# Optimization experiments

Hardware: AMD Instinct MI355X
Metric: run time of the kernel (lower is better)

## Reference

```python
import jax, jax.numpy as jnp
import numpy as np

N_USERS = 1024
N_ITEMS = 2048
N = N_USERS + N_ITEMS          # 3072 total nodes
D = 128                        # latent_dim_rec
L = 3                          # n_layers
K = [64, 64, 64]               # top-k per layer for getMaskAdj
GAMMA = 0.2                    # residual weight on svd embeddings
X_SCALE = 1.0                  # delta
B = 8192                       # batch of (user, item) pairs


def setup_inputs() -> dict:
    key = jax.random.key(0)
    ks = jax.random.split(key, 9)
    # normalized-adjacency-like dense graph: nonnegative, row sums ~ 1
    A = jax.random.uniform(ks[0], (N, N), dtype=jnp.float32) * (2.0 / N)
    user_emb = jax.random.normal(ks[1], (N_USERS, D), dtype=jnp.float32)
    item_emb = jax.random.normal(ks[2], (N_ITEMS, D), dtype=jnp.float32)
    user_emb0 = jax.random.normal(ks[3], (N_USERS, D), dtype=jnp.float32)
    item_emb0 = jax.random.normal(ks[4], (N_ITEMS, D), dtype=jnp.float32)
    vector_u = jax.random.uniform(ks[5], (1, N), dtype=jnp.float32)
    vector_v = jax.random.uniform(ks[6], (1, N), dtype=jnp.float32)
    users = jax.random.randint(ks[7], (B,), 0, N_USERS)
    items = jax.random.randint(ks[8], (B,), 0, N_ITEMS)
    return {
        "users": users, "items": items, "A": A,
        "user_emb": user_emb, "item_emb": item_emb,
        "user_emb0": user_emb0, "item_emb0": item_emb0,
        "vector_u": vector_u, "vector_v": vector_v,
    }


def topk_mask(M, k):
    """Keep top-k entries per row of M, zero elsewhere (getMaskAdj)."""
    vals, idx = jax.lax.top_k(M, k)          # [N,k], [N,k]
    rows = jnp.arange(M.shape[0])[:, None]
    return jnp.zeros_like(M).at[rows, idx].set(vals)


def _computer(A, user_emb, item_emb, user_emb0, item_emb0, vector_u, vector_v):
    all_emb = jnp.concatenate([user_emb, item_emb], axis=0)      # [N,D]
    all_emb0 = jnp.concatenate([user_emb0, item_emb0], axis=0)   # [N,D]
    u = vector_u[0]  # [N]
    v = vector_v[0]  # [N]

    # ---- computAttention: w_k = u A^k v for k = 0..L (A^0 = I via A_0=eye) ----
    w_list = [jnp.dot(u, v)]
    powers = []           # A^1 .. A^L (g_droped progression)
    Ak = A
    for layer in range(L):
        powers.append(Ak)
        w_list.append(jnp.dot(u, Ak @ v))
        if layer < L - 1:
            Ak = A @ Ak   # g_droped = Graph @ A_k
    w = jnp.stack(w_list)                 # [L+1]
    w = w / jnp.sum(w)
    attention_weight = jax.nn.softmax(w)  # softmax(dim=0)

    # ---- getMaskAdj: top-k masked powers ----
    A_list = [topk_mask(powers[l], K[l]) if K[l] != 0 else powers[l] for l in range(L)]

    # ---- layer-wise propagation with attention-weighted accumulation ----
    emb0 = all_emb
    light_out = X_SCALE * attention_weight[0] * all_emb
    for layer in range(L):
        e = A_list[layer] @ emb0 + GAMMA * all_emb0   # SpMM + residual
        light_out = light_out + X_SCALE * attention_weight[layer + 1] * e
    users_all = light_out[:N_USERS]
    items_all = light_out[N_USERS:]
    return users_all, items_all


def reference(users, items, A, user_emb, item_emb, user_emb0, item_emb0, vector_u, vector_v):
    users_all, items_all = _computer(A, user_emb, item_emb, user_emb0, item_emb0, vector_u, vector_v)
    u_e = users_all[users]   # [B,D]
    i_e = items_all[items]   # [B,D]
    return jnp.sum(u_e * i_e, axis=1)  # [B]
```

## Files before the change

### kernel.cpp

```cpp
#include <hip/hip_runtime.h>
#include <hip/hip_fp8.h>
#include <math.h>

#define NN 3072
#define NU 1024
#define NI 2048
#define DD 128
#define BB 8192
#define GAMMA_F 0.2f

#define SCALE_A 524288.0f
#define F8SCALE2 1.9073486328125e-06f
#define DESCALE38 3.637978807091713e-12f

#define KBLK ((size_t)NN * 64)

typedef __attribute__((ext_vector_type(4))) float f32x4;
typedef __attribute__((ext_vector_type(16))) float f32x16;
typedef __attribute__((ext_vector_type(4))) int i32x4;
typedef __attribute__((ext_vector_type(8))) int i32x8;

static __device__ inline unsigned short bf16bits(float x) {
  union { unsigned u; float f; } cv;
  cv.f = x;
  unsigned r = cv.u + 0x7fff + ((cv.u >> 16) & 1);
  return (unsigned short)(r >> 16);
}

static __device__ inline unsigned pk4_f8(float a, float b, float c, float d) {
#if defined(__has_builtin)
#if __has_builtin(__builtin_amdgcn_cvt_pk_fp8_f32)
  int p = __builtin_amdgcn_cvt_pk_fp8_f32(a, b, 0, false);
  p = __builtin_amdgcn_cvt_pk_fp8_f32(c, d, p, true);
  return (unsigned)p;
#else
  return (unsigned)__hip_fp8_e4m3(a).__x | ((unsigned)__hip_fp8_e4m3(b).__x << 8) |
         ((unsigned)__hip_fp8_e4m3(c).__x << 16) |
         ((unsigned)__hip_fp8_e4m3(d).__x << 24);
#endif
#else
  return (unsigned)__hip_fp8_e4m3(a).__x | ((unsigned)__hip_fp8_e4m3(b).__x << 8) |
         ((unsigned)__hip_fp8_e4m3(c).__x << 16) |
         ((unsigned)__hip_fp8_e4m3(d).__x << 24);
#endif
}

static __device__ inline void atomAddF(float* p, float v) {
#if defined(__has_builtin)
#if __has_builtin(__builtin_amdgcn_global_atomic_fadd_f32)
  __builtin_amdgcn_global_atomic_fadd_f32(
      (__attribute__((address_space(1))) float*)p, v);
#else
  unsafeAtomicAdd(p, v);
#endif
#else
  unsafeAtomicAdd(p, v);
#endif
}

static __device__ inline float block_sum(float s, float* red4) {
  int tid = threadIdx.x;
  for (int off = 32; off; off >>= 1) s += __shfl_down(s, off, 64);
  if ((tid & 63) == 0) red4[tid >> 6] = s;
  __syncthreads();
  return red4[0] + red4[1] + red4[2] + red4[3];
}

static __device__ inline float row_dot_f32(const float* __restrict__ a,
                                           const float* __restrict__ b,
                                           float* red4) {
  const float4* ap = (const float4*)a;
  const float4* bp = (const float4*)b;
  float s = 0.f;
  for (int j = threadIdx.x; j < NN / 4; j += 256) {
    float4 x = ap[j], y = bp[j];
    s += x.x * y.x + x.y * y.y + x.z * y.z + x.w * y.w;
  }
  return block_sum(s, red4);
}

static __device__ inline void load48_bf(const unsigned short* __restrict__ b0,
                                        int parts, int row, int lane,
                                        float* f) {
  const uint4* r0 = (const uint4*)(b0 + (size_t)row * NN);
#pragma unroll
  for (int j = 0; j < 6; ++j) {
    uint4 q = r0[lane + j * 64];
    unsigned uu[4] = {q.x, q.y, q.z, q.w};
#pragma unroll
    for (int e = 0; e < 4; ++e) {
      f[j * 8 + e * 2] = __uint_as_float(uu[e] << 16);
      f[j * 8 + e * 2 + 1] = __uint_as_float(uu[e] & 0xffff0000u);
    }
  }
  for (int p = 1; p < parts; ++p) {
    const uint4* rp = (const uint4*)(b0 + (size_t)p * NN * NN + (size_t)row * NN);
#pragma unroll
    for (int j = 0; j < 6; ++j) {
      uint4 q = rp[lane + j * 64];
      unsigned uu[4] = {q.x, q.y, q.z, q.w};
#pragma unroll
      for (int e = 0; e < 4; ++e) {
        f[j * 8 + e * 2] += __uint_as_float(uu[e] << 16);
        f[j * 8 + e * 2 + 1] += __uint_as_float(uu[e] & 0xffff0000u);
      }
    }
  }
}

static __device__ inline void load48_f32(const float* __restrict__ A, int row,
                                         int lane, float* f) {
  const float4* r0 = (const float4*)(A + (size_t)row * NN);
#pragma unroll
  for (int j = 0; j < 12; ++j) {
    float4 a = r0[lane + j * 64];
    f[j * 4 + 0] = a.x; f[j * 4 + 1] = a.y;
    f[j * 4 + 2] = a.z; f[j * 4 + 3] = a.w;
  }
}

static __device__ void select_compact(const float* f, int lane, float descale,
                                      int bf, int* __restrict__ outCnt,
                                      int* __restrict__ outIdx,
                                      float* __restrict__ outVal) {
  unsigned bor = 0, band = 0xffffffffu;
#pragma unroll
  for (int r = 0; r < 48; ++r) {
    unsigned k = __float_as_uint(f[r]);
    bor |= k; band &= k;
  }
  for (int off = 32; off; off >>= 1) {
    bor |= (unsigned)__shfl_xor((int)bor, off, 64);
    band &= (unsigned)__shfl_xor((int)band, off, 64);
  }
  unsigned diff = bor ^ band;
  int hi = diff ? (31 - __clz(diff)) : 16;
  if (hi < 16) hi = 16;
  if (hi > 30) hi = 30;
  unsigned t = band & ~((2u << hi) - 1u);

  int b = hi;
  while (b >= 17) {
    unsigned base = 1u << (b - 1);
    unsigned cand1 = t | base;
    unsigned cand2 = t | (base << 1);
    unsigned cand3 = cand2 | base;
    int c1 = 0, c2 = 0, c3 = 0;
#pragma unroll
    for (int r = 0; r < 48; ++r) {
      unsigned k = __float_as_uint(f[r]);
      c1 += (k >= cand1) ? 1 : 0;
      c2 += (k >= cand2) ? 1 : 0;
      c3 += (k >= cand3) ? 1 : 0;
    }
    for (int off = 32; off; off >>= 1) {
      c1 += __shfl_xor(c1, off, 64);
      c2 += __shfl_xor(c2, off, 64);
      c3 += __shfl_xor(c3, off, 64);
    }
    if (c3 >= 64) t = cand3;
    else if (c2 >= 64) t = cand2;
    else if (c1 >= 64) t = cand1;
    b -= 2;
  }
  if (b == 16) {
    unsigned cand = t | (1u << 16);
    int c = 0;
#pragma unroll
    for (int r = 0; r < 48; ++r) c += (__float_as_uint(f[r]) >= cand) ? 1 : 0;
    for (int off = 32; off; off >>= 1) c += __shfl_xor(c, off, 64);
    if (c >= 64) t = cand;
  }

  int basec = 0;
#pragma unroll
  for (int r = 0; r < 48; ++r) {
    bool keep = __float_as_uint(f[r]) >= t;
    unsigned long long m = __ballot(keep);
    if (keep) {
      int pos = basec + __popcll(m & ((1ull << lane) - 1ull));
      if (pos < 128) {
        int col = bf ? ((r >> 3) * 512 + lane * 8 + (r & 7))
                     : ((r >> 2) * 256 + lane * 4 + (r & 3));
        outIdx[pos] = col << 7;
        outVal[pos] = f[r] * descale;
      }
    }
    basec += __popcll(m);
  }
  if (lane == 0) *outCnt = basec < 128 ? basec : 128;
}

__global__ __launch_bounds__(256) void prep(
    const float* __restrict__ A, const float* __restrict__ vu,
    const float* __restrict__ vv, unsigned char* __restrict__ Af8,
    unsigned char* __restrict__ Atf8, float* __restrict__ y1,
    float* __restrict__ s1, const float* __restrict__ uemb,
    const float* __restrict__ iemb, float* __restrict__ allE) {
  __shared__ float sh[64 * 65 + 512];
  const int bid = blockIdx.x;
  const int t = threadIdx.x;
  if (bid >= 2304) {
    int idx = (bid - 2304) * 256 + t;
    int e = idx * 4;
    float4 v = (e < NU * DD) ? *(const float4*)(uemb + e)
                             : *(const float4*)(iemb + (e - NU * DD));
    *(float4*)(allE + e) = v;
    return;
  }
  const int bx = (bid % 48) * 64, by = (bid / 48) * 64;
  const int rr = t >> 4;
  const int c4 = (t & 15) * 4;
  for (int it = 0; it < 4; ++it) {
    int r = rr + it * 16;
    float4 val = *(const float4*)(A + (size_t)(by + r) * NN + bx + c4);
    sh[r * 65 + c4] = val.x; sh[r * 65 + c4 + 1] = val.y;
    sh[r * 65 + c4 + 2] = val.z; sh[r * 65 + c4 + 3] = val.w;
  }
  __syncthreads();
  {
    int row = t >> 2, ch = t & 3;
    const float* sp = &sh[row * 65 + ch * 16];
    uint4 w;
    w.x = pk4_f8(sp[0] * SCALE_A, sp[1] * SCALE_A, sp[2] * SCALE_A,
                 sp[3] * SCALE_A);
    w.y = pk4_f8(sp[4] * SCALE_A, sp[5] * SCALE_A, sp[6] * SCALE_A,
                 sp[7] * SCALE_A);
    w.z = pk4_f8(sp[8] * SCALE_A, sp[9] * SCALE_A, sp[10] * SCALE_A,
                 sp[11] * SCALE_A);
    w.w = pk4_f8(sp[12] * SCALE_A, sp[13] * SCALE_A, sp[14] * SCALE_A,
                 sp[15] * SCALE_A);
    *(uint4*)(Af8 + (size_t)(bx >> 6) * KBLK + (size_t)(by + row) * 64 +
              ch * 16) = w;
  }
  {
    int c = t >> 2, ch = t & 3;
    float v[16];
#pragma unroll
    for (int e = 0; e < 16; ++e) v[e] = sh[(ch * 16 + e) * 65 + c];
    uint4 w;
    w.x = pk4_f8(v[0] * SCALE_A, v[1] * SCALE_A, v[2] * SCALE_A,
                 v[3] * SCALE_A);
    w.y = pk4_f8(v[4] * SCALE_A, v[5] * SCALE_A, v[6] * SCALE_A,
                 v[7] * SCALE_A);
    w.z = pk4_f8(v[8] * SCALE_A, v[9] * SCALE_A, v[10] * SCALE_A,
                 v[11] * SCALE_A);
    w.w = pk4_f8(v[12] * SCALE_A, v[13] * SCALE_A, v[14] * SCALE_A,
                 v[15] * SCALE_A);
    *(uint4*)(Atf8 + (size_t)(by >> 6) * KBLK + (size_t)(bx + c) * 64 +
              ch * 16) = w;
  }
  const int q = t >> 6;
  const int l = t & 63;
  float sy = 0.f, ss_ = 0.f;
  for (int i = 0; i < 16; ++i) {
    int c = q * 16 + i;
    sy += sh[l * 65 + c] * vv[bx + c];
    ss_ += vu[by + c] * sh[c * 65 + l];
  }
  float* red = sh + 64 * 65;
  red[q * 64 + l] = sy;
  red[256 + q * 64 + l] = ss_;
  __syncthreads();
  if (t < 64) {
    float v4 = red[t] + red[64 + t] + red[128 + t] + red[192 + t];
    atomAddF(&y1[by + t], v4);
  } else if (t < 128) {
    int cc = t - 64;
    float v4 = red[256 + cc] + red[256 + 64 + cc] + red[256 + 128 + cc] +
               red[256 + 192 + cc];
    atomAddF(&s1[bx + cc], v4);
  }
}

static __device__ inline i32x8 ldfragL(const char* p) {
  i32x4 lo = *(const i32x4*)p;
  i32x4 hi = *(const i32x4*)(p + 1024);
  return (i32x8){lo.x, lo.y, lo.z, lo.w, hi.x, hi.y, hi.z, hi.w};
}

__global__ __launch_bounds__(256) void gemm_f8(
    const unsigned char* __restrict__ Ag,
    const unsigned char* __restrict__ Btg,
    unsigned short* __restrict__ Cg) {
  __shared__ char smem[3][24576];
  const int wg = blockIdx.x;
  const int xcd = wg & 7;
  const int idx = wg >> 3;
  const int bxi = xcd * 2 + (idx & 1);
  const int byi = idx >> 1;
  const int rowBase = byi * 192, colBase = bxi * 192;

  const int t = threadIdx.x;
  const int w = t >> 6, l = t & 63;
  const int wr = w >> 1, wc = w & 1;
  const int r32 = l & 31, hh = l >> 5;

  f32x16 acc[3][3];
#pragma unroll
  for (int i = 0; i < 3; ++i)
#pragma unroll
    for (int j = 0; j < 3; ++j)
#pragma unroll
      for (int e = 0; e < 16; ++e) acc[i][j][e] = 0.f;

  const unsigned char* aT = Ag + (size_t)rowBase * 64;
  const unsigned char* bT = Btg + (size_t)colBase * 64;
  const int laneOff = r32 * 64 + hh * 32;

#define STAGE(kt, b)                                                        \
  {                                                                         \
    const size_t kOff = (size_t)(kt) * KBLK;                                \
    _Pragma("unroll") for (int r_ = 0; r_ < 6; ++r_) {                      \
      int q_ = r_ * 4 + w;                                                  \
      int qq_ = q_ < 12 ? q_ : q_ - 12;                                     \
      int s_ = qq_ >> 1, h_ = qq_ & 1;                                      \
      const unsigned char* g_ = ((q_ < 12) ? aT : bT) + kOff +              \
                                (size_t)(s_ * 32) * 64 + laneOff + h_ * 16; \
      __builtin_amdgcn_global_load_lds(                                     \
          (const __attribute__((address_space(1))) unsigned*)g_,            \
          (__attribute__((address_space(3))) unsigned*)(smem[b] +           \
                                                        q_ * 1024),         \
          16, 0, 0);                                                        \
    }                                                                       \
  }

  const int nt = NN / 64;
  STAGE(0, 0);
  STAGE(1, 1);
  for (int kt = 0; kt < nt; ++kt) {
    if (kt < nt - 1) {
      asm volatile("s_waitcnt vmcnt(6)" ::: "memory");
    } else {
      asm volatile("s_waitcnt vmcnt(0)" ::: "memory");
    }
    __builtin_amdgcn_s_barrier();
    __builtin_amdgcn_sched_barrier(0);
    const char* sb = smem[kt % 3];
    i32x8 af[3], bfr[3];
#pragma unroll
    for (int i = 0; i < 3; ++i)
      af[i] = ldfragL(sb + (wr * 3 + i) * 2048 + l * 16);
#pragma unroll
    for (int j = 0; j < 3; ++j)
      bfr[j] = ldfragL(sb + 12288 + (wc * 3 + j) * 2048 + l * 16);
    if (kt + 2 < nt) STAGE(kt + 2, (kt + 2) % 3);
    __builtin_amdgcn_s_setprio(1);
#pragma unroll
    for (int i = 0; i < 3; ++i)
#pragma unroll
      for (int j = 0; j < 3; ++j)
        acc[i][j] = __builtin_amdgcn_mfma_scale_f32_32x32x64_f8f6f4(
            af[i], bfr[j], acc[i][j], 0, 0, 0, 127, 0, 127);
    __builtin_amdgcn_s_setprio(0);
    __builtin_amdgcn_sched_barrier(0);
  }
#undef STAGE

#pragma unroll
  for (int i = 0; i < 3; ++i) {
    int rb = rowBase + wr * 96 + i * 32 + 4 * hh;
#pragma unroll
    for (int j = 0; j < 3; ++j) {
      int cc = colBase + wc * 96 + j * 32 + r32;
#pragma unroll
      for (int reg = 0; reg < 16; ++reg) {
        int rr = rb + (reg & 3) + 8 * (reg >> 2);
        Cg[(size_t)rr * NN + cc] = bf16bits(acc[i][j][reg]);
      }
    }
  }
}

__global__ __launch_bounds__(256) void post1(
    const unsigned short* __restrict__ C, int parts,
    const float* __restrict__ A, const float* __restrict__ y1,
    unsigned char* __restrict__ A2f8, int* __restrict__ cnts1,
    int* __restrict__ tIdx1, float* __restrict__ tVal1,
    float* __restrict__ tvec) {
  const int bid = blockIdx.x;
  const int t = threadIdx.x;
  if (bid < 768) {
    int row = bid * 4 + (t >> 6);
    int lane = t & 63;
    float f[48];
    load48_bf(C, parts, row, lane, f);
#pragma unroll
    for (int j = 0; j < 6; ++j) {
      uint2 w;
      w.x = pk4_f8(f[j * 8 + 0] * F8SCALE2, f[j * 8 + 1] * F8SCALE2,
                   f[j * 8 + 2] * F8SCALE2, f[j * 8 + 3] * F8SCALE2);
      w.y = pk4_f8(f[j * 8 + 4] * F8SCALE2, f[j * 8 + 5] * F8SCALE2,
                   f[j * 8 + 6] * F8SCALE2, f[j * 8 + 7] * F8SCALE2);
      size_t addr = (size_t)(j * 8 + (lane >> 3)) * KBLK +
                    (size_t)row * 64 + (lane & 7) * 8;
      *(uint2*)(A2f8 + addr) = w;
    }
    select_compact(f, lane, DESCALE38, 1, &cnts1[row],
                   tIdx1 + (size_t)row * 128, tVal1 + (size_t)row * 128);
  } else {
    int row = (bid - 768) * 4 + (t >> 6);
    int lane = t & 63;
    const float4* rp = (const float4*)(A + (size_t)row * NN);
    const float4* yp = (const float4*)y1;
    float s = 0.f;
#pragma unroll
    for (int j = 0; j < 12; ++j) {
      float4 a = rp[lane + j * 64];
      float4 y = yp[lane + j * 64];
      s += a.x * y.x + a.y * y.y + a.z * y.z + a.w * y.w;
    }
    for (int off = 32; off; off >>= 1) s += __shfl_down(s, off, 64);
    if (lane == 0) tvec[row] = s;
  }
}

__global__ __launch_bounds__(256) void sel02(
    const unsigned short* __restrict__ C, int parts,
    const float* __restrict__ A, int* __restrict__ cnt0,
    int* __restrict__ idx0, float* __restrict__ val0,
    int* __restrict__ cnt2, int* __restrict__ idx2,
    float* __restrict__ val2, const float* __restrict__ vu,
    const float* __restrict__ vv, const float* __restrict__ y1,
    const float* __restrict__ s1, const float* __restrict__ tvec,
    float* __restrict__ wacc) {
  __shared__ float red4[4];
  const int bid = blockIdx.x;
  const int t = threadIdx.x;
  if (bid == 1536) {
    float w0 = row_dot_f32(vu, vv, red4);  __syncthreads();
    float w1 = row_dot_f32(vu, y1, red4);  __syncthreads();
    float w2 = row_dot_f32(s1, y1, red4);  __syncthreads();
    float w3 = row_dot_f32(s1, tvec, red4);
    if (t == 0) { wacc[0] = w0; wacc[1] = w1; wacc[2] = w2; wacc[3] = w3; }
    return;
  }
  const int w = t >> 6, lane = t & 63;
  const int row = (bid >> 1) * 4 + w;
  float f[48];
  if ((bid & 1) == 0) {
    load48_bf(C, parts, row, lane, f);
    select_compact(f, lane, DESCALE38, 1, &cnt2[row],
                   idx2 + (size_t)row * 128, val2 + (size_t)row * 128);
  } else {
    load48_f32(A, row, lane, f);
    select_compact(f, lane, 1.0f, 0, &cnt0[row],
                   idx0 + (size_t)row * 128, val0 + (size_t)row * 128);
  }
}

__global__ __launch_bounds__(256) void gather_light(
    const float* __restrict__ allE, const float* __restrict__ uemb0,
    const float* __restrict__ iemb0, const float* __restrict__ wacc,
    const int* __restrict__ cnt0, const int* __restrict__ idx0,
    const float* __restrict__ val0, const int* __restrict__ cnts1,
    const int* __restrict__ tIdx1, const float* __restrict__ tVal1,
    const int* __restrict__ cnt2, const int* __restrict__ idx2,
    const float* __restrict__ val2, float* __restrict__ lightOut) {
  __shared__ int li[4][384];
  __shared__ float lv[4][384];
  const int t = threadIdx.x;
  const int w = t >> 6, lane = t & 63;
  const int row = blockIdx.x * 4 + w;

  float w0 = wacc[0], w1 = wacc[1], w2 = wacc[2], w3 = wacc[3];
  float ss = w0 + w1 + w2 + w3;
  w0 /= ss; w1 /= ss; w2 /= ss; w3 /= ss;
  float m = fmaxf(fmaxf(w0, w1), fmaxf(w2, w3));
  float ex0 = expf(w0 - m), ex1 = expf(w1 - m), ex2 = expf(w2 - m),
        ex3 = expf(w3 - m);
  float se = ex0 + ex1 + ex2 + ex3;
  float aw0 = ex0 / se, aw1 = ex1 / se, aw2 = ex2 / se, aw3 = ex3 / se;
  float aw4 = GAMMA_F * (aw1 + aw2 + aw3);

  const int c0 = cnt0[row], c1 = cnts1[row], c2 = cnt2[row];
  const int p0 = (c0 + 7) & ~7, p1 = (c1 + 7) & ~7, p2 = (c2 + 7) & ~7;
  int* Li = li[w];
  float* Lv = lv[w];
  const size_t rb = (size_t)row * 128;
  for (int k = lane; k < p0; k += 64) {
    bool in = k < c0;
    Li[k] = in ? idx0[rb + k] : 0;
    Lv[k] = in ? aw1 * val0[rb + k] : 0.f;
  }
  for (int k = lane; k < p1; k += 64) {
    bool in = k < c1;
    Li[p0 + k] = in ? tIdx1[rb + k] : 0;
    Lv[p0 + k] = in ? aw2 * tVal1[rb + k] : 0.f;
  }
  for (int k = lane; k < p2; k += 64) {
    bool in = k < c2;
    Li[p0 + p1 + k] = in ? idx2[rb + k] : 0;
    Lv[p0 + p1 + k] = in ? aw3 * val2[rb + k] : 0.f;
  }

  const int ct = p0 + p1 + p2;
  const float2* E2 = (const float2*)allE;
  float ax = 0.f, ay = 0.f, bx_ = 0.f, by_ = 0.f;
  for (int k = 0; k < ct; k += 8) {
    int i0 = Li[k + 0], i1 = Li[k + 1], i2 = Li[k + 2], i3 = Li[k + 3];
    int i4 = Li[k + 4], i5 = Li[k + 5], i6 = Li[k + 6], i7 = Li[k + 7];
    float v0 = Lv[k + 0], v1 = Lv[k + 1], v2 = Lv[k + 2], v3 = Lv[k + 3];
    float v4 = Lv[k + 4], v5 = Lv[k + 5], v6 = Lv[k + 6], v7 = Lv[k + 7];
    float2 g0 = E2[(i0 >> 1) + lane];
    float2 g1 = E2[(i1 >> 1) + lane];
    float2 g2 = E2[(i2 >> 1) + lane];
    float2 g3 = E2[(i3 >> 1) + lane];
    float2 g4 = E2[(i4 >> 1) + lane];
    float2 g5 = E2[(i5 >> 1) + lane];
    float2 g6 = E2[(i6 >> 1) + lane];
    float2 g7 = E2[(i7 >> 1) + lane];
    ax += v0 * g0.x; ay += v0 * g0.y;
    bx_ += v1 * g1.x; by_ += v1 * g1.y;
    ax += v2 * g2.x; ay += v2 * g2.y;
    bx_ += v3 * g3.x; by_ += v3 * g3.y;
    ax += v4 * g4.x; ay += v4 * g4.y;
    bx_ += v5 * g5.x; by_ += v5 * g5.y;
    ax += v6 * g6.x; ay += v6 * g6.y;
    bx_ += v7 * g7.x; by_ += v7 * g7.y;
  }
  float2 sE = E2[((size_t)row << 6) + lane];
  float2 e0 = (row < NU)
                  ? ((const float2*)uemb0)[(size_t)row * 64 + lane]
                  : ((const float2*)iemb0)[(size_t)(row - NU) * 64 + lane];
  float ox = (ax + bx_) + aw0 * sE.x + aw4 * e0.x;
  float oy = (ay + by_) + aw0 * sE.y + aw4 * e0.y;
  float2 o; o.x = ox; o.y = oy;
  ((float2*)lightOut)[(size_t)row * 64 + lane] = o;
}

__global__ __launch_bounds__(256) void out_dot(const int* __restrict__ users,
                                               const int* __restrict__ items,
                                               const float* __restrict__ lightOut,
                                               float* __restrict__ out) {
  int b = blockIdx.x * 4 + (threadIdx.x >> 6);
  int lane = threadIdx.x & 63;
  const float* up = lightOut + (size_t)users[b] * DD;
  const float* ip = lightOut + (size_t)(NU + items[b]) * DD;
  float s = up[lane] * ip[lane] + up[lane + 64] * ip[lane + 64];
  for (int off = 32; off; off >>= 1) s += __shfl_down(s, off, 64);
  if (lane == 0) out[b] = s;
}

extern "C" void kernel_launch(void* const* d_in, const int* in_sizes, int n_in,
                              void* d_out, int out_size, void* d_ws,
                              size_t ws_size, hipStream_t stream) {
  const int* users = (const int*)d_in[0];
  const int* items = (const int*)d_in[1];
  const float* A = (const float*)d_in[2];
  const float* uemb = (const float*)d_in[3];
  const float* iemb = (const float*)d_in[4];
  const float* uemb0 = (const float*)d_in[5];
  const float* iemb0 = (const float*)d_in[6];
  const float* vu = (const float*)d_in[7];
  const float* vv = (const float*)d_in[8];
  float* out = (float*)d_out;

  char* ws = (char*)d_ws;
  size_t off = 0;
  auto alloc = [&](size_t bytes) -> void* {
    void* p = ws + off;
    off += (bytes + 255) & ~(size_t)255;
    return p;
  };
  unsigned char* Af8 = (unsigned char*)alloc((size_t)NN * NN);
  unsigned char* Atf8 = (unsigned char*)alloc((size_t)NN * NN);
  unsigned char* A2f8 = (unsigned char*)alloc((size_t)NN * NN);
  float* y1 = (float*)alloc((size_t)NN * 4);
  float* s1 = (float*)alloc((size_t)NN * 4);
  float* tvec = (float*)alloc((size_t)NN * 4);
  float* wacc = (float*)alloc(256);
  int* cnts1 = (int*)alloc((size_t)NN * 4);
  int* tIdx1 = (int*)alloc((size_t)NN * 128 * 4);
  float* tVal1 = (float*)alloc((size_t)NN * 128 * 4);
  float* lightOut = (float*)alloc((size_t)NN * DD * 4);
  int* cnt0 = (int*)alloc((size_t)NN * 4);
  int* cnt2 = (int*)alloc((size_t)NN * 4);
  float* allE = (float*)alloc((size_t)NN * DD * 4);

  const size_t LSTB = (size_t)NN * 128 * 4;
  int* idx0 = (int*)(Atf8);
  float* val0 = (float*)(Atf8 + LSTB);
  int* idx2 = (int*)(Atf8 + 2 * LSTB);
  float* val2 = (float*)(Atf8 + 3 * LSTB);

  unsigned short* C = (unsigned short*)alloc((size_t)NN * NN * 2);

  hipMemsetAsync(y1, 0, (size_t)2 * NN * 4, stream);
  prep<<<2688, 256, 0, stream>>>(A, vu, vv, Af8, Atf8, y1, s1, uemb, iemb,
                                 allE);
  gemm_f8<<<256, 256, 0, stream>>>(Af8, Atf8, C);
  post1<<<1536, 256, 0, stream>>>(C, 1, A, y1, A2f8, cnts1, tIdx1, tVal1,
                                  tvec);
  gemm_f8<<<256, 256, 0, stream>>>(A2f8, Atf8, C);
  sel02<<<1537, 256, 0, stream>>>(C, 1, A, cnt0, idx0, val0, cnt2, idx2,
                                  val2, vu, vv, y1, s1, tvec, wacc);
  gather_light<<<768, 256, 0, stream>>>(allE, uemb0, iemb0, wacc, cnt0, idx0,
                                        val0, cnts1, tIdx1, tVal1, cnt2, idx2,
                                        val2, lightOut);
  out_dot<<<BB / 4, 256, 0, stream>>>(users, items, lightOut, out);
}
```

Measured before the change: 239.9 us.

## Split K across two wave groups in FP8 GEMM with LDS reduction

The FP8 GEMM block grows from 4 to 8 waves. Two groups of four waves each handle alternating 64-wide K tiles with their own triple-buffered LDS staging. At the end, the second group writes its accumulators to shared memory and the first group adds them before storing bf16 output. This raises the number of waves per CU to hide memory and MFMA latency, since there are only 256 blocks. The cost is doubled LDS use (about 144KB per block), a barrier-synchronised reduction through LDS, and higher register pressure under launch_bounds 512.

```diff
diff --git a/kernel.cpp b/kernel.cpp
--- a/kernel.cpp
+++ b/kernel.cpp
@@ -279,11 +279,11 @@
   return (i32x8){lo.x, lo.y, lo.z, lo.w, hi.x, hi.y, hi.z, hi.w};
 }
 
-__global__ __launch_bounds__(256) void gemm_f8(
+__global__ __launch_bounds__(512) void gemm_f8(
     const unsigned char* __restrict__ Ag,
     const unsigned char* __restrict__ Btg,
     unsigned short* __restrict__ Cg) {
-  __shared__ char smem[3][24576];
+  __shared__ char smem[2][3][24576];
   const int wg = blockIdx.x;
   const int xcd = wg & 7;
   const int idx = wg >> 3;
@@ -293,7 +293,9 @@
 
   const int t = threadIdx.x;
   const int w = t >> 6, l = t & 63;
-  const int wr = w >> 1, wc = w & 1;
+  const int kp = w >> 2;
+  const int wq = w & 3;
+  const int wr = wq >> 1, wc = wq & 1;
   const int r32 = l & 31, hh = l >> 5;
 
   f32x16 acc[3][3];
@@ -312,61 +314,85 @@
   {                                                                         \
     const size_t kOff = (size_t)(kt) * KBLK;                                \
     _Pragma("unroll") for (int r_ = 0; r_ < 6; ++r_) {                      \
-      int q_ = r_ * 4 + w;                                                  \
+      int q_ = r_ * 4 + wq;                                                 \
       int qq_ = q_ < 12 ? q_ : q_ - 12;                                     \
       int s_ = qq_ >> 1, h_ = qq_ & 1;                                      \
       const unsigned char* g_ = ((q_ < 12) ? aT : bT) + kOff +              \
                                 (size_t)(s_ * 32) * 64 + laneOff + h_ * 16; \
       __builtin_amdgcn_global_load_lds(                                     \
           (const __attribute__((address_space(1))) unsigned*)g_,            \
-          (__attribute__((address_space(3))) unsigned*)(smem[b] +           \
+          (__attribute__((address_space(3))) unsigned*)(smem[kp][b] +       \
                                                         q_ * 1024),         \
           16, 0, 0);                                                        \
     }                                                                       \
   }
 
-  const int nt = NN / 64;
-  STAGE(0, 0);
-  STAGE(1, 1);
-  for (int kt = 0; kt < nt; ++kt) {
-    if (kt < nt - 1) {
+  const int ni = 24;
+  STAGE(kp, 0);
+  STAGE(2 + kp, 1);
+  for (int i = 0; i < ni; ++i) {
+    if (i < ni - 1) {
       asm volatile("s_waitcnt vmcnt(6)" ::: "memory");
     } else {
       asm volatile("s_waitcnt vmcnt(0)" ::: "memory");
     }
     __builtin_amdgcn_s_barrier();
     __builtin_amdgcn_sched_barrier(0);
-    const char* sb = smem[kt % 3];
+    const char* sb = smem[kp][i % 3];
     i32x8 af[3], bfr[3];
 #pragma unroll
-    for (int i = 0; i < 3; ++i)
-      af[i] = ldfragL(sb + (wr * 3 + i) * 2048 + l * 16);
+    for (int ii = 0; ii < 3; ++ii)
+      af[ii] = ldfragL(sb + (wr * 3 + ii) * 2048 + l * 16);
 #pragma unroll
     for (int j = 0; j < 3; ++j)
       bfr[j] = ldfragL(sb + 12288 + (wc * 3 + j) * 2048 + l * 16);
-    if (kt + 2 < nt) STAGE(kt + 2, (kt + 2) % 3);
+    if (i + 2 < ni) STAGE(2 * (i + 2) + kp, (i + 2) % 3);
     __builtin_amdgcn_s_setprio(1);
 #pragma unroll
-    for (int i = 0; i < 3; ++i)
+    for (int ii = 0; ii < 3; ++ii)
 #pragma unroll
       for (int j = 0; j < 3; ++j)
-        acc[i][j] = __builtin_amdgcn_mfma_scale_f32_32x32x64_f8f6f4(
-            af[i], bfr[j], acc[i][j], 0, 0, 0, 127, 0, 127);
+        acc[ii][j] = __builtin_amdgcn_mfma_scale_f32_32x32x64_f8f6f4(
+            af[ii], bfr[j], acc[ii][j], 0, 0, 0, 127, 0, 127);
     __builtin_amdgcn_s_setprio(0);
     __builtin_amdgcn_sched_barrier(0);
   }
 #undef STAGE
 
-#pragma unroll
-  for (int i = 0; i < 3; ++i) {
-    int rb = rowBase + wr * 96 + i * 32 + 4 * hh;
-#pragma unroll
-    for (int j = 0; j < 3; ++j) {
-      int cc = colBase + wc * 96 + j * 32 + r32;
-#pragma unroll
-      for (int reg = 0; reg < 16; ++reg) {
-        int rr = rb + (reg & 3) + 8 * (reg >> 2);
-        Cg[(size_t)rr * NN + cc] = bf16bits(acc[i][j][reg]);
+  float* mbase = (float*)&smem[0][0][0];
+  if (kp == 1) {
+    float* dst = mbase + (size_t)wq * 9216;
+#pragma unroll
+    for (int i = 0; i < 3; ++i)
+#pragma unroll
+      for (int j = 0; j < 3; ++j) {
+        float* p = dst + (i * 3 + j) * 1024 + l * 16;
+#pragma unroll
+        for (int e = 0; e < 16; ++e) p[e] = acc[i][j][e];
+      }
+  }
+  __syncthreads();
+  if (kp == 0) {
+    const float* src = mbase + (size_t)wq * 9216;
+#pragma unroll
+    for (int i = 0; i < 3; ++i)
+#pragma unroll
+      for (int j = 0; j < 3; ++j) {
+        const float* p = src + (i * 3 + j) * 1024 + l * 16;
+#pragma unroll
+        for (int e = 0; e < 16; ++e) acc[i][j][e] += p[e];
+      }
+#pragma unroll
+    for (int i = 0; i < 3; ++i) {
+      int rb = rowBase + wr * 96 + i * 32 + 4 * hh;
+#pragma unroll
+      for (int j = 0; j < 3; ++j) {
+        int cc = colBase + wc * 96 + j * 32 + r32;
+#pragma unroll
+        for (int reg = 0; reg < 16; ++reg) {
+          int rr = rb + (reg & 3) + 8 * (reg >> 2);
+          Cg[(size_t)rr * NN + cc] = bf16bits(acc[i][j][reg]);
+        }
       }
     }
   }
@@ -589,10 +615,10 @@
   hipMemsetAsync(y1, 0, (size_t)2 * NN * 4, stream);
   prep<<<2688, 256, 0, stream>>>(A, vu, vv, Af8, Atf8, y1, s1, uemb, iemb,
                                  allE);
-  gemm_f8<<<256, 256, 0, stream>>>(Af8, Atf8, C);
+  gemm_f8<<<256, 512, 0, stream>>>(Af8, Atf8, C);
   post1<<<1536, 256, 0, stream>>>(C, 1, A, y1, A2f8, cnts1, tIdx1, tVal1,
                                   tvec);
-  gemm_f8<<<256, 256, 0, stream>>>(A2f8, Atf8, C);
+  gemm_f8<<<256, 512, 0, stream>>>(A2f8, Atf8, C);
   sel02<<<1537, 256, 0, stream>>>(C, 1, A, cnt0, idx0, val0, cnt2, idx2,
                                   val2, vu, vv, y1, s1, tvec, wacc);
   gather_light<<<768, 256, 0, stream>>>(allE, uemb0, iemb0, wacc, cnt0, idx0,
```

Result: no change. 240.2 us (+0.1%).

## Split FP8 GEMM K dimension in two to double workgroup count

Applied to the files above, without the earlier changes.

The FP8 matrix-power GEMM now splits the 3072-long K loop into two halves, launching 512 workgroups instead of 256. Each half writes its own bf16 partial result buffer, and the consumer kernels sum the two parts. The goal is to fill more of the GPU's compute units, since 256 workgroups underuse the device. In exchange it doubles the intermediate C memory traffic and adds rounding of two bf16 partials. Launch bounds are also raised to two blocks per CU.

```diff
diff --git a/kernel.cpp b/kernel.cpp
--- a/kernel.cpp
+++ b/kernel.cpp
@@ -279,7 +279,7 @@
   return (i32x8){lo.x, lo.y, lo.z, lo.w, hi.x, hi.y, hi.z, hi.w};
 }
 
-__global__ __launch_bounds__(256) void gemm_f8(
+__global__ __launch_bounds__(256, 2) void gemm_f8(
     const unsigned char* __restrict__ Ag,
     const unsigned char* __restrict__ Btg,
     unsigned short* __restrict__ Cg) {
@@ -288,7 +288,8 @@
   const int xcd = wg & 7;
   const int idx = wg >> 3;
   const int bxi = xcd * 2 + (idx & 1);
-  const int byi = idx >> 1;
+  const int byi = (idx >> 1) & 15;
+  const int z = idx >> 5;
   const int rowBase = byi * 192, colBase = bxi * 192;
 
   const int t = threadIdx.x;
@@ -307,6 +308,7 @@
   const unsigned char* aT = Ag + (size_t)rowBase * 64;
   const unsigned char* bT = Btg + (size_t)colBase * 64;
   const int laneOff = r32 * 64 + hh * 32;
+  const int kt0 = z * 24;
 
 #define STAGE(kt, b)                                                        \
   {                                                                         \
@@ -325,38 +327,39 @@
     }                                                                       \
   }
 
-  const int nt = NN / 64;
-  STAGE(0, 0);
-  STAGE(1, 1);
-  for (int kt = 0; kt < nt; ++kt) {
-    if (kt < nt - 1) {
+  const int ni = 24;
+  STAGE(kt0, 0);
+  STAGE(kt0 + 1, 1);
+  for (int i = 0; i < ni; ++i) {
+    if (i < ni - 1) {
       asm volatile("s_waitcnt vmcnt(6)" ::: "memory");
     } else {
       asm volatile("s_waitcnt vmcnt(0)" ::: "memory");
     }
     __builtin_amdgcn_s_barrier();
     __builtin_amdgcn_sched_barrier(0);
-    const char* sb = smem[kt % 3];
+    const char* sb = smem[i % 3];
     i32x8 af[3], bfr[3];
 #pragma unroll
-    for (int i = 0; i < 3; ++i)
-      af[i] = ldfragL(sb + (wr * 3 + i) * 2048 + l * 16);
+    for (int ii = 0; ii < 3; ++ii)
+      af[ii] = ldfragL(sb + (wr * 3 + ii) * 2048 + l * 16);
 #pragma unroll
     for (int j = 0; j < 3; ++j)
       bfr[j] = ldfragL(sb + 12288 + (wc * 3 + j) * 2048 + l * 16);
-    if (kt + 2 < nt) STAGE(kt + 2, (kt + 2) % 3);
+    if (i + 2 < ni) STAGE(kt0 + i + 2, (i + 2) % 3);
     __builtin_amdgcn_s_setprio(1);
 #pragma unroll
-    for (int i = 0; i < 3; ++i)
+    for (int ii = 0; ii < 3; ++ii)
 #pragma unroll
       for (int j = 0; j < 3; ++j)
-        acc[i][j] = __builtin_amdgcn_mfma_scale_f32_32x32x64_f8f6f4(
-            af[i], bfr[j], acc[i][j], 0, 0, 0, 127, 0, 127);
+        acc[ii][j] = __builtin_amdgcn_mfma_scale_f32_32x32x64_f8f6f4(
+            af[ii], bfr[j], acc[ii][j], 0, 0, 0, 127, 0, 127);
     __builtin_amdgcn_s_setprio(0);
     __builtin_amdgcn_sched_barrier(0);
   }
 #undef STAGE
 
+  unsigned short* Cout = Cg + (size_t)z * NN * NN;
 #pragma unroll
   for (int i = 0; i < 3; ++i) {
     int rb = rowBase + wr * 96 + i * 32 + 4 * hh;
@@ -366,7 +369,7 @@
 #pragma unroll
       for (int reg = 0; reg < 16; ++reg) {
         int rr = rb + (reg & 3) + 8 * (reg >> 2);
-        Cg[(size_t)rr * NN + cc] = bf16bits(acc[i][j][reg]);
+        Cout[(size_t)rr * NN + cc] = bf16bits(acc[i][j][reg]);
       }
     }
   }
@@ -584,16 +587,16 @@
   int* idx2 = (int*)(Atf8 + 2 * LSTB);
   float* val2 = (float*)(Atf8 + 3 * LSTB);
 
-  unsigned short* C = (unsigned short*)alloc((size_t)NN * NN * 2);
+  unsigned short* C = (unsigned short*)alloc((size_t)2 * NN * NN * 2);
 
   hipMemsetAsync(y1, 0, (size_t)2 * NN * 4, stream);
   prep<<<2688, 256, 0, stream>>>(A, vu, vv, Af8, Atf8, y1, s1, uemb, iemb,
                                  allE);
-  gemm_f8<<<256, 256, 0, stream>>>(Af8, Atf8, C);
-  post1<<<1536, 256, 0, stream>>>(C, 1, A, y1, A2f8, cnts1, tIdx1, tVal1,
+  gemm_f8<<<512, 256, 0, stream>>>(Af8, Atf8, C);
+  post1<<<1536, 256, 0, stream>>>(C, 2, A, y1, A2f8, cnts1, tIdx1, tVal1,
                                   tvec);
-  gemm_f8<<<256, 256, 0, stream>>>(A2f8, Atf8, C);
-  sel02<<<1537, 256, 0, stream>>>(C, 1, A, cnt0, idx0, val0, cnt2, idx2,
+  gemm_f8<<<512, 256, 0, stream>>>(A2f8, Atf8, C);
+  sel02<<<1537, 256, 0, stream>>>(C, 2, A, cnt0, idx0, val0, cnt2, idx2,
                                   val2, vu, vv, y1, s1, tvec, wacc);
   gather_light<<<768, 256, 0, stream>>>(allE, uemb0, iemb0, wacc, cnt0, idx0,
                                         val0, cnts1, tIdx1, tVal1, cnt2, idx2,
```

New measurement: 238.1 us. No clear change (-0.7%).
